# Kernel tuning notes

Hardware: AMD Instinct MI355X
Metric: run time of the kernel (lower is better)

## Reference

```python
import jax, jax.numpy as jnp
import numpy as np

N = 50000      # n_nodes
E = 800000     # edges (before self-loops)
IN = 128       # in_dim
HID = 32       # hidden_dim (per-head out channels)
HEADS = 4
EMB = 128      # embed_dim
LAYERS = 3
NEG_SLOPE = 0.2  # PyG GATv2 default leaky_relu slope


def _layer_norm(x, g, b):
    mu = jnp.mean(x, axis=-1, keepdims=True)
    var = jnp.var(x, axis=-1, keepdims=True)
    return g * (x - mu) / jnp.sqrt(var + 1e-5) + b


def _gatv2(h, src, dst, n, Wl, bl, Wr, br, att, bias):
    # GATv2Conv (PyG semantics, share_weights=False, concat=True).
    H, C = att.shape
    xl = (h @ Wl + bl).reshape(n, H, C)   # target (i) transform
    xr = (h @ Wr + br).reshape(n, H, C)   # source (j) transform
    x_i = xl[dst]                          # [Etot, H, C] gather
    x_j = xr[src]
    e = jax.nn.leaky_relu(x_i + x_j, NEG_SLOPE)
    logit = jnp.einsum('ehc,hc->eh', e, att)          # [Etot, H]
    # segment softmax over destination node (every node has a self-loop)
    m = jax.ops.segment_max(logit, dst, num_segments=n)
    ex = jnp.exp(logit - m[dst])
    den = jax.ops.segment_sum(ex, dst, num_segments=n)
    alpha = ex / (den[dst] + 1e-16)
    out = jax.ops.segment_sum(alpha[..., None] * x_j, dst, num_segments=n)
    return out.reshape(n, H * C) + bias


def setup_inputs() -> dict:
    key = jax.random.key(0)
    ks = iter(jax.random.split(key, 64))
    d = {}
    d['x'] = jax.random.normal(next(ks), (N, IN), jnp.float32)
    d['edge_index'] = jax.random.randint(next(ks), (2, E), 0, N, dtype=jnp.int64)

    def w(shape, fan):
        return jax.random.normal(next(ks), shape, jnp.float32) / np.float32(np.sqrt(fan))

    HC = HID * HEADS
    d['W_in'] = w((IN, HID), IN); d['b_in'] = jnp.zeros((HID,), jnp.float32)
    for i in range(LAYERS):
        ic = HID if i == 0 else HC
        d[f'Wl{i}'] = w((ic, HC), ic); d[f'bl{i}'] = jnp.zeros((HC,), jnp.float32)
        d[f'Wr{i}'] = w((ic, HC), ic); d[f'br{i}'] = jnp.zeros((HC,), jnp.float32)
        d[f'att{i}'] = w((HEADS, HID), HID)
        d[f'bo{i}'] = jnp.zeros((HC,), jnp.float32)
        d[f'g{i}'] = jnp.ones((HC,), jnp.float32)
        d[f'be{i}'] = jnp.zeros((HC,), jnp.float32)
    d['W_out'] = w((HC, EMB), HC); d['b_out'] = jnp.zeros((EMB,), jnp.float32)
    return d


def reference(x, edge_index, W_in, b_in,
              Wl0, bl0, Wr0, br0, att0, bo0, g0, be0,
              Wl1, bl1, Wr1, br1, att1, bo1, g1, be1,
              Wl2, bl2, Wr2, br2, att2, bo2, g2, be2,
              W_out, b_out):
    n = x.shape[0]
    loops = jnp.arange(n, dtype=edge_index.dtype)  # add_self_loops=True
    src = jnp.concatenate([edge_index[0], loops])
    dst = jnp.concatenate([edge_index[1], loops])

    h = jax.nn.gelu(x @ W_in + b_in, approximate=False)
    layers = [(Wl0, bl0, Wr0, br0, att0, bo0, g0, be0),
              (Wl1, bl1, Wr1, br1, att1, bo1, g1, be1),
              (Wl2, bl2, Wr2, br2, att2, bo2, g2, be2)]
    for (Wl, bl, Wr, br, att, bo, g, be) in layers:
        h_new = jax.nn.gelu(_layer_norm(_gatv2(h, src, dst, n, Wl, bl, Wr, br, att, bo), g, be), approximate=False)
        h = h + h_new if h.shape == h_new.shape else h_new  # dropout = identity (eval)
    out = h @ W_out + b_out
    norm = jnp.maximum(jnp.linalg.norm(out, axis=-1, keepdims=True), 1e-12)
    return out / norm
```

## Files before the change

### kernel.cpp

```cpp
#include <hip/hip_runtime.h>
#include <hip/hip_bf16.h>
#include <math.h>

#define N_NODES 50000
#define N_EDGES 800000
#define IN_DIM  128
#define HC_DIM  128
#define HID_C   32
#define SCAN_NB 196
#define LOG2E   1.4426950408889634f

typedef __attribute__((ext_vector_type(8))) short short8;
typedef __attribute__((ext_vector_type(4))) short short4v;
typedef __attribute__((ext_vector_type(4))) float f32x4;
typedef _Float16 hf8 __attribute__((ext_vector_type(8)));
typedef _Float16 hf2 __attribute__((ext_vector_type(2)));
typedef unsigned int uint4v __attribute__((ext_vector_type(4)));

__device__ __forceinline__ float gelu_f(float x){
    return 0.5f*x*(1.0f + erff(x*0.7071067811865475f));
}

__device__ __forceinline__ void split2(float f, short& h, short& l){
    __hip_bfloat16 bh = __float2bfloat16(f);
    float r = f - __bfloat162float(bh);
    __hip_bfloat16 blo = __float2bfloat16(r);
    h = *reinterpret_cast<short*>(&bh);
    l = *reinterpret_cast<short*>(&blo);
}
__device__ __forceinline__ unsigned short f2h(float f){
    _Float16 h = (_Float16)f;
    return __builtin_bit_cast(unsigned short, h);
}

__global__ __launch_bounds__(256) void k_count(const int* __restrict__ dst, int* __restrict__ cnt,
                                               int* __restrict__ rank){
    int b = blockIdx.x*1024 + threadIdx.x;
    #pragma unroll
    for(int i=0;i<4;i++){
        int e = b + i*256;
        if(e < N_EDGES) rank[e] = atomicAdd(&cnt[dst[e]], 1);
    }
}

__global__ __launch_bounds__(256) void k_scan1(const int* __restrict__ cnt, int* __restrict__ rowptr,
                                               int* __restrict__ part){
    __shared__ int sh[256];
    int t=threadIdx.x; int i=blockIdx.x*256+t;
    int v = (i<N_NODES)? cnt[i] : 0;
    sh[t]=v; __syncthreads();
    for(int off=1; off<256; off<<=1){
        int y = (t>=off)? sh[t-off] : 0;
        __syncthreads();
        sh[t] += y;
        __syncthreads();
    }
    if(i<N_NODES) rowptr[i] = sh[t]-v;
    if(t==255) part[blockIdx.x] = sh[255];
}

__global__ __launch_bounds__(256) void k_scan2(int* __restrict__ part){
    __shared__ int sh[256];
    int t=threadIdx.x;
    int v = (t<SCAN_NB)? part[t] : 0;
    sh[t]=v; __syncthreads();
    for(int off=1; off<256; off<<=1){
        int y=(t>=off)? sh[t-off]:0;
        __syncthreads();
        sh[t]+=y;
        __syncthreads();
    }
    if(t<SCAN_NB) part[t] = sh[t]-v;
}

__global__ __launch_bounds__(256) void k_scan3(int* __restrict__ rowptr, const int* __restrict__ part){
    int t=threadIdx.x; int i=blockIdx.x*256+t;
    if(i<N_NODES) rowptr[i] += part[blockIdx.x];
    if(i==0) rowptr[N_NODES]=N_EDGES;
}

__global__ __launch_bounds__(256) void k_fill(const int* __restrict__ src, const int* __restrict__ dst,
                                              const int* __restrict__ rowptr, const int* __restrict__ rank,
                                              int* __restrict__ col){
    int b = blockIdx.x*1024 + threadIdx.x;
    #pragma unroll
    for(int i=0;i<4;i++){
        int e = b + i*256;
        if(e < N_EDGES) col[rowptr[dst[e]] + rank[e]] = src[e];
    }
}

__global__ __launch_bounds__(256) void k_splitW(const float* __restrict__ W0, const float* __restrict__ W1,
                                                const float* __restrict__ W2, const float* __restrict__ W3,
                                                const float* __restrict__ W4, const float* __restrict__ W5,
                                                const float* __restrict__ W6, short* __restrict__ WT){
    int bx = blockIdx.x;
    int m, kc;
    if(bx < 2){ m = bx; kc = 0; }
    else { m = 2 + (bx-2)/4; kc = (bx-2)&3; }
    const float* src; int K; size_t off;
    switch(m){
        case 0: src=W0; K=32;  off=0;      break;
        case 1: src=W1; K=32;  off=8192;   break;
        case 2: src=W2; K=128; off=16384;  break;
        case 3: src=W3; K=128; off=49152;  break;
        case 4: src=W4; K=128; off=81920;  break;
        case 5: src=W5; K=128; off=114688; break;
        default:src=W6; K=128; off=147456; break;
    }
    short* hi = WT + off;
    short* lo = hi + (size_t)K*HC_DIM;
    #pragma unroll
    for(int i=0;i<16;i++){
        int idx = threadIdx.x + i*256;
        int k = kc*32 + (idx>>7);
        int n = idx & 127;
        float f = src[(size_t)k*HC_DIM + n];
        short h,l; split2(f,h,l);
        hi[(size_t)n*K + k] = h;
        lo[(size_t)n*K + k] = l;
    }
}

__global__ __launch_bounds__(256) void k_gemm_in(const float* __restrict__ x, const float* __restrict__ W,
                                                 const float* __restrict__ b, float* __restrict__ h,
                                                 short* __restrict__ hhi, short* __restrict__ hlo){
    int id = blockIdx.x*256+threadIdx.x;
    int r = id>>5, c = id&31;
    const float4* x4 = (const float4*)(x + (size_t)r*IN_DIM);
    float acc=0.f;
    #pragma unroll 8
    for(int k=0;k<IN_DIM/4;k++){
        float4 xv = x4[k];
        acc = fmaf(xv.x, W[(4*k  )*HID_C+c], acc);
        acc = fmaf(xv.y, W[(4*k+1)*HID_C+c], acc);
        acc = fmaf(xv.z, W[(4*k+2)*HID_C+c], acc);
        acc = fmaf(xv.w, W[(4*k+3)*HID_C+c], acc);
    }
    float v = gelu_f(acc + b[c]);
    h[(size_t)r*HID_C+c] = v;
    short hh,ll; split2(v,hh,ll);
    hhi[(size_t)r*HID_C+c] = hh;
    hlo[(size_t)r*HID_C+c] = ll;
}

template<int K, bool PAIR, bool NORM>
__global__ __launch_bounds__(256) void k_mfma(const short* __restrict__ Ahi, const short* __restrict__ Alo,
                                              const short* __restrict__ WTl, const float* __restrict__ bl,
                                              const short* __restrict__ WTr, const float* __restrict__ br,
                                              float* __restrict__ XL, unsigned short* __restrict__ XR16){
    constexpr int LDS_K = 40;
    constexpr int NCH = K / 32;
    __shared__ short As_hi[64*LDS_K], As_lo[64*LDS_K];
    __shared__ short Bh0[128*LDS_K], Bl0[128*LDS_K];
    __shared__ short Bh1[PAIR?128*LDS_K:1], Bl1[PAIR?128*LDS_K:1];
    __shared__ float ssq[NORM?256:1];

    int t = threadIdx.x;
    int lane = t & 63, wave = t >> 6;
    int quad = lane >> 4, ml = lane & 15;
    int rbase = blockIdx.x * 64;

    const short* WTl_lo = WTl + (size_t)K*HC_DIM;
    const short* WTr_lo = PAIR ? (WTr + (size_t)K*HC_DIM) : nullptr;

    f32x4 accL[4][2], accR[4][2];
    #pragma unroll
    for(int i=0;i<4;i++)
        #pragma unroll
        for(int j=0;j<2;j++){ accL[i][j]=(f32x4){0,0,0,0}; accR[i][j]=(f32x4){0,0,0,0}; }

    int r = t >> 2, seg = t & 3;
    int gr = rbase + r; if(gr >= N_NODES) gr = N_NODES-1;

    for(int c=0; c<NCH; c++){
        if(c) __syncthreads();
        size_t ka = (size_t)gr*K + c*32 + seg*8;
        *(short8*)(As_hi + r*LDS_K + seg*8) = *(const short8*)(Ahi + ka);
        *(short8*)(As_lo + r*LDS_K + seg*8) = *(const short8*)(Alo + ka);
        #pragma unroll
        for(int u=0; u<2; u++){
            int uu = t + u*256;
            int n = uu >> 2, sg = uu & 3;
            size_t kw = (size_t)n*K + c*32 + sg*8;
            *(short8*)(Bh0 + n*LDS_K + sg*8) = *(const short8*)(WTl + kw);
            *(short8*)(Bl0 + n*LDS_K + sg*8) = *(const short8*)(WTl_lo + kw);
            if(PAIR){
                *(short8*)(Bh1 + n*LDS_K + sg*8) = *(const short8*)(WTr + kw);
                *(short8*)(Bl1 + n*LDS_K + sg*8) = *(const short8*)(WTr_lo + kw);
            }
        }
        __syncthreads();

        int k0 = quad*8;
        short8 ah[4], al[4];
        #pragma unroll
        for(int i=0;i<4;i++){
            ah[i] = *(const short8*)(As_hi + (16*i + ml)*LDS_K + k0);
            al[i] = *(const short8*)(As_lo + (16*i + ml)*LDS_K + k0);
        }
        #pragma unroll
        for(int j=0;j<2;j++){
            int nrow = j*64 + wave*16 + ml;
            short8 bh = *(const short8*)(Bh0 + nrow*LDS_K + k0);
            short8 blo = *(const short8*)(Bl0 + nrow*LDS_K + k0);
            #pragma unroll
            for(int i=0;i<4;i++){
                accL[i][j] = __builtin_amdgcn_mfma_f32_16x16x32_bf16(ah[i], bh,  accL[i][j], 0,0,0);
                accL[i][j] = __builtin_amdgcn_mfma_f32_16x16x32_bf16(ah[i], blo, accL[i][j], 0,0,0);
                accL[i][j] = __builtin_amdgcn_mfma_f32_16x16x32_bf16(al[i], bh,  accL[i][j], 0,0,0);
            }
            if(PAIR){
                short8 ch = *(const short8*)(Bh1 + nrow*LDS_K + k0);
                short8 cl = *(const short8*)(Bl1 + nrow*LDS_K + k0);
                #pragma unroll
                for(int i=0;i<4;i++){
                    accR[i][j] = __builtin_amdgcn_mfma_f32_16x16x32_bf16(ah[i], ch, accR[i][j], 0,0,0);
                    accR[i][j] = __builtin_amdgcn_mfma_f32_16x16x32_bf16(ah[i], cl, accR[i][j], 0,0,0);
                    accR[i][j] = __builtin_amdgcn_mfma_f32_16x16x32_bf16(al[i], ch, accR[i][j], 0,0,0);
                }
            }
        }
    }

    int col0 = wave*16 + ml, col1 = 64 + wave*16 + ml;
    float bL0 = bl[col0], bL1 = bl[col1];

    if(NORM){
        #pragma unroll
        for(int i=0;i<4;i++){
            #pragma unroll
            for(int rr=0;rr<4;rr++){
                float v0 = accL[i][0][rr] + bL0;
                float v1 = accL[i][1][rr] + bL1;
                float p = v0*v0 + v1*v1;
                p += __shfl_xor(p,1); p += __shfl_xor(p,2);
                p += __shfl_xor(p,4); p += __shfl_xor(p,8);
                if(ml==0) ssq[wave*64 + 16*i + quad*4 + rr] = p;
            }
        }
        __syncthreads();
        #pragma unroll
        for(int i=0;i<4;i++){
            #pragma unroll
            for(int rr=0;rr<4;rr++){
                int row = 16*i + quad*4 + rr;
                int grr = rbase + row;
                if(grr < N_NODES){
                    float tot = ssq[row] + ssq[64+row] + ssq[128+row] + ssq[192+row];
                    float inv = 1.0f / fmaxf(sqrtf(tot), 1e-12f);
                    XL[(size_t)grr*HC_DIM + col0] = (accL[i][0][rr] + bL0) * inv;
                    XL[(size_t)grr*HC_DIM + col1] = (accL[i][1][rr] + bL1) * inv;
                }
            }
        }
    } else {
        float bR0 = PAIR ? br[col0] : 0.f, bR1 = PAIR ? br[col1] : 0.f;
        #pragma unroll
        for(int i=0;i<4;i++){
            #pragma unroll
            for(int rr=0;rr<4;rr++){
                int grr = rbase + 16*i + quad*4 + rr;
                if(grr < N_NODES){
                    XL[(size_t)grr*HC_DIM + col0] = accL[i][0][rr] + bL0;
                    XL[(size_t)grr*HC_DIM + col1] = accL[i][1][rr] + bL1;
                    if(PAIR){
                        XR16[(size_t)grr*HC_DIM + col0] = f2h(accR[i][0][rr] + bR0);
                        XR16[(size_t)grr*HC_DIM + col1] = f2h(accR[i][1][rr] + bR1);
                    }
                }
            }
        }
    }
}

__global__ __launch_bounds__(256) void k_node(const float* __restrict__ XL, const unsigned short* __restrict__ XR,
    const int* __restrict__ rowptr, const int* __restrict__ colidx,
    const float* __restrict__ att, const float* __restrict__ bo,
    const float* __restrict__ gg, const float* __restrict__ be,
    const float* __restrict__ hold, float* __restrict__ hout,
    short* __restrict__ hi_out, short* __restrict__ lo_out)
{
    int wave=threadIdx.x>>6, lane=threadIdx.x&63;
    int node = blockIdx.x*4+wave;
    int qd = lane >> 4, cl = lane & 15;
    int c8 = cl << 3;

    const float* xlp = XL + (size_t)node*HC_DIM + c8;
    float4 xa = *(const float4*)xlp;
    float4 xb = *(const float4*)(xlp+4);
    float xlf[8] = {xa.x,xa.y,xa.z,xa.w,xb.x,xb.y,xb.z,xb.w};
    float4 aa = *(const float4*)(att + c8);
    float4 abv = *(const float4*)(att + c8 + 4);
    float af[8] = {aa.x,aa.y,aa.z,aa.w,abv.x,abv.y,abv.z,abv.w};
    hf8 xlh, av6, av4;
    const float s6 = 0.6f*LOG2E, s4 = 0.4f*LOG2E;
    #pragma unroll
    for(int k=0;k<8;k++){
        xlh[k] = (_Float16)xlf[k];
        av6[k] = (_Float16)(af[k]*s6);
        av4[k] = (_Float16)(af[k]*s4);
    }

    int beg = rowptr[node], end = rowptr[node+1];

    #define H2(v,k) __builtin_shufflevector(v, v, 2*(k), 2*(k)+1)
    #define LOADH(j, xv) { xv = *(const hf8*)((const _Float16*)XR + ((size_t)((unsigned)(j)<<7)) + c8); }
#if defined(__has_builtin) && __has_builtin(__builtin_amdgcn_fdot2)
    #define LOGIT(xv, q) { \
        hf8 u_ = xlh + xv; \
        hf8 a_ = __builtin_bit_cast(hf8, __builtin_bit_cast(uint4v, u_) & 0x7fff7fffu); \
        float qa_ = __builtin_amdgcn_fdot2(H2(u_,0), H2(av6,0), 0.f, false); \
        float qb_ = __builtin_amdgcn_fdot2(H2(a_,0), H2(av4,0), 0.f, false); \
        qa_ = __builtin_amdgcn_fdot2(H2(u_,1), H2(av6,1), qa_, false); \
        qb_ = __builtin_amdgcn_fdot2(H2(a_,1), H2(av4,1), qb_, false); \
        qa_ = __builtin_amdgcn_fdot2(H2(u_,2), H2(av6,2), qa_, false); \
        qb_ = __builtin_amdgcn_fdot2(H2(a_,2), H2(av4,2), qb_, false); \
        qa_ = __builtin_amdgcn_fdot2(H2(u_,3), H2(av6,3), qa_, false); \
        qb_ = __builtin_amdgcn_fdot2(H2(a_,3), H2(av4,3), qb_, false); \
        q = qa_ + qb_; \
        q += __shfl_xor(q,1); q += __shfl_xor(q,2); }
#else
    #define LOGIT(xv, q) { \
        hf8 u_ = xlh + xv; \
        hf8 a_ = __builtin_bit_cast(hf8, __builtin_bit_cast(uint4v, u_) & 0x7fff7fffu); \
        q = 0.f; \
        _Pragma("unroll") \
        for(int k_=0;k_<8;k_++) q = fmaf((float)u_[k_], (float)av6[k_], fmaf((float)a_[k_], (float)av4[k_], q)); \
        q += __shfl_xor(q,1); q += __shfl_xor(q,2); }
#endif
    #define UPDATE4 { \
        float nm = fmaxf(m, fmaxf(fmaxf(q0,q1),fmaxf(q2,q3))); \
        float sc = exp2f(m-nm); \
        float e0=exp2f(q0-nm), e1=exp2f(q1-nm), e2=exp2f(q2-nm), e3=exp2f(q3-nm); \
        ls = fmaf(ls, sc, (e0+e1)+(e2+e3)); \
        _Pragma("unroll") \
        for(int k=0;k<8;k++) \
            acc[k] = fmaf(acc[k], sc, fmaf(e0,(float)x0[k], fmaf(e1,(float)x1[k], fmaf(e2,(float)x2[k], e3*(float)x3[k])))); \
        m = nm; }

    hf8 xs; LOADH(node, xs)
    float qs; LOGIT(xs, qs)
    float m, ls, acc[8];
    if(qd==0){
        m = qs; ls = 1.f;
        #pragma unroll
        for(int k=0;k<8;k++) acc[k] = (float)xs[k];
    } else {
        m = -1e30f; ls = 0.f;
        #pragma unroll
        for(int k=0;k<8;k++) acc[k] = 0.f;
    }

    int P = end - beg;
    int nb = P >> 4;
    int base = beg;
    int qoff = qd << 2;
    for(int b=0; b<nb; b++, base += 16){
        int b2 = base + qoff;
        int j0 = colidx[b2], j1 = colidx[b2+1], j2 = colidx[b2+2], j3 = colidx[b2+3];
        hf8 x0,x1,x2,x3;
        LOADH(j0,x0) LOADH(j1,x1) LOADH(j2,x2) LOADH(j3,x3)
        float q0,q1,q2,q3;
        LOGIT(x0,q0) LOGIT(x1,q1) LOGIT(x2,q2) LOGIT(x3,q3)
        UPDATE4
    }
    if(base < end){
        int b2 = base + qoff;
        int j0 = (b2  <end)? colidx[b2]   : node;
        int j1 = (b2+1<end)? colidx[b2+1] : node;
        int j2 = (b2+2<end)? colidx[b2+2] : node;
        int j3 = (b2+3<end)? colidx[b2+3] : node;
        hf8 x0,x1,x2,x3;
        LOADH(j0,x0) LOADH(j1,x1) LOADH(j2,x2) LOADH(j3,x3)
        float q0,q1,q2,q3;
        LOGIT(x0,q0) LOGIT(x1,q1) LOGIT(x2,q2) LOGIT(x3,q3)
        if(b2+1>=end) q1 = -INFINITY;
        if(b2+2>=end) q2 = -INFINITY;
        if(b2+3>=end) q3 = -INFINITY;
        if(b2 < end){
            UPDATE4
        }
    }
    #undef UPDATE4
    #undef LOGIT
    #undef LOADH
    #undef H2

    #pragma unroll
    for(int mk=16; mk<=32; mk<<=1){
        float mo  = __shfl_xor(m, mk);
        float lso = __shfl_xor(ls, mk);
        float ao[8];
        #pragma unroll
        for(int k=0;k<8;k++) ao[k] = __shfl_xor(acc[k], mk);
        float nm = fmaxf(m, mo);
        float s0 = exp2f(m-nm), s1 = exp2f(mo-nm);
        ls = ls*s0 + lso*s1;
        #pragma unroll
        for(int k=0;k<8;k++) acc[k] = acc[k]*s0 + ao[k]*s1;
        m = nm;
    }

    float inv = 1.0f/ls;
    float4 b0 = *(const float4*)(bo + c8);
    float4 b1 = *(const float4*)(bo + c8 + 4);
    float bof[8] = {b0.x,b0.y,b0.z,b0.w,b1.x,b1.y,b1.z,b1.w};
    float o[8];
    #pragma unroll
    for(int k=0;k<8;k++) o[k] = fmaf(acc[k], inv, bof[k]);
    float s1v = ((o[0]+o[1])+(o[2]+o[3])) + ((o[4]+o[5])+(o[6]+o[7]));
    float s2v = o[0]*o[0];
    #pragma unroll
    for(int k=1;k<8;k++) s2v = fmaf(o[k],o[k],s2v);
    #pragma unroll
    for(int mk=1;mk<16;mk<<=1){ s1v += __shfl_xor(s1v,mk); s2v += __shfl_xor(s2v,mk); }
    float mean = s1v*(1.f/128.f);
    float var  = s2v*(1.f/128.f) - mean*mean;
    float rstd = rsqrtf(var + 1e-5f);

    int ch2 = c8 + (qd<<1);
    float oa = (qd&2) ? ((qd&1)? o[6] : o[4]) : ((qd&1)? o[2] : o[0]);
    float ob = (qd&2) ? ((qd&1)? o[7] : o[5]) : ((qd&1)? o[3] : o[1]);
    float2 g2  = *(const float2*)(gg + ch2);
    float2 be2 = *(const float2*)(be + ch2);
    float r0 = gelu_f(fmaf(g2.x*(oa-mean), rstd, be2.x));
    float r1 = gelu_f(fmaf(g2.y*(ob-mean), rstd, be2.y));
    if(hold){
        float2 hv = *(const float2*)(hold + (size_t)node*HC_DIM + ch2);
        r0 += hv.x; r1 += hv.y;
    }
    *(float2*)(hout + (size_t)node*HC_DIM + ch2) = make_float2(r0,r1);
    short h0,l0,h1,l1;
    split2(r0,h0,l0); split2(r1,h1,l1);
    *(short2*)(hi_out + (size_t)node*HC_DIM + ch2) = make_short2(h0,h1);
    *(short2*)(lo_out + (size_t)node*HC_DIM + ch2) = make_short2(l0,l1);
}

extern "C" void kernel_launch(void* const* d_in, const int* in_sizes, int n_in,
                              void* d_out, int out_size, void* d_ws, size_t ws_size,
                              hipStream_t stream)
{
    const float* x   = (const float*)d_in[0];
    const int*   ei  = (const int*)  d_in[1];
    const float* Win = (const float*)d_in[2];
    const float* bin = (const float*)d_in[3];
    const float *Wl[3], *bl[3], *Wr[3], *br[3], *att[3], *bo[3], *gg[3], *be[3];
    for(int i=0;i<3;i++){
        const int base = 4 + 8*i;
        Wl[i]=(const float*)d_in[base+0]; bl[i]=(const float*)d_in[base+1];
        Wr[i]=(const float*)d_in[base+2]; br[i]=(const float*)d_in[base+3];
        att[i]=(const float*)d_in[base+4]; bo[i]=(const float*)d_in[base+5];
        gg[i]=(const float*)d_in[base+6]; be[i]=(const float*)d_in[base+7];
    }
    const float* Wout=(const float*)d_in[28];
    const float* bout=(const float*)d_in[29];
    float* out = (float*)d_out;

    char* w = (char*)d_ws;
    float* hA = (float*)w;  w += (size_t)N_NODES*HC_DIM*4;
    float* hB = (float*)w;  w += (size_t)N_NODES*HC_DIM*4;
    float* XL = (float*)w;  w += (size_t)N_NODES*HC_DIM*4;
    unsigned short* XR16 = (unsigned short*)w; w += (size_t)N_NODES*HC_DIM*2;
    short* hAhi = (short*)w; w += (size_t)N_NODES*HC_DIM*2;
    short* hAlo = (short*)w; w += (size_t)N_NODES*HC_DIM*2;
    short* hBhi = (short*)w; w += (size_t)N_NODES*HC_DIM*2;
    short* hBlo = (short*)w; w += (size_t)N_NODES*HC_DIM*2;
    short* WT   = (short*)w; w += (size_t)180224*2;
    int* rowptr = (int*)w;  w += (size_t)(N_NODES+2)*4;
    int* cursor = (int*)w;  w += (size_t)N_NODES*4;
    int* colidx = (int*)w;  w += (size_t)N_EDGES*4;
    int* rank   = (int*)w;  w += (size_t)N_EDGES*4;
    int* part   = (int*)w;  w += 256*4;

    const int* srcp = ei;
    const int* dstp = ei + N_EDGES;

    const short* WTl0 = WT + 0;      const short* WTr0 = WT + 8192;
    const short* WTl1 = WT + 16384;  const short* WTr1 = WT + 49152;
    const short* WTl2 = WT + 81920;  const short* WTr2 = WT + 114688;
    const short* WTo  = WT + 147456;

    k_splitW<<<22,256,0,stream>>>(Wl[0],Wr[0],Wl[1],Wr[1],Wl[2],Wr[2],Wout, WT);
    hipMemsetAsync(cursor, 0, (size_t)N_NODES*4, stream);
    k_count <<<782,256, 0, stream>>>(dstp, cursor, rank);
    k_scan1 <<<SCAN_NB,256,0,stream>>>(cursor, rowptr, part);
    k_scan2 <<<1,   256, 0, stream>>>(part);
    k_scan3 <<<SCAN_NB,256,0,stream>>>(rowptr, part);
    k_fill  <<<782,256, 0, stream>>>(srcp, dstp, rowptr, rank, colidx);
    k_gemm_in<<<6250,256,0,stream>>>(x, Win, bin, hA, hAhi, hAlo);

    k_mfma<32,true,false><<<782,256,0,stream>>>(hAhi, hAlo, WTl0, bl[0], WTr0, br[0], XL, XR16);
    k_node<<<12500,256,0,stream>>>(XL,XR16,rowptr,colidx,att[0],bo[0],gg[0],be[0],
                                   (const float*)nullptr, hB, hBhi, hBlo);

    k_mfma<128,true,false><<<782,256,0,stream>>>(hBhi, hBlo, WTl1, bl[1], WTr1, br[1], XL, XR16);
    k_node<<<12500,256,0,stream>>>(XL,XR16,rowptr,colidx,att[1],bo[1],gg[1],be[1], hB, hA, hAhi, hAlo);

    k_mfma<128,true,false><<<782,256,0,stream>>>(hAhi, hAlo, WTl2, bl[2], WTr2, br[2], XL, XR16);
    k_node<<<12500,256,0,stream>>>(XL,XR16,rowptr,colidx,att[2],bo[2],gg[2],be[2], hA, hB, hBhi, hBlo);

    k_mfma<128,false,true><<<782,256,0,stream>>>(hBhi, hBlo, WTo, bout, nullptr, nullptr, out, nullptr);
}
```

Baseline: 496.6 us.

## Drop fp32 hidden buffers, store XL as fp16, add low-degree single-pass softmax path

The fp32 copies of the hidden state are removed. The residual is rebuilt from the bf16 hi/lo split arrays, and the XL projection is written as fp16 instead of fp32, which cuts global writes and reads in every layer. k_node also gets a new path for nodes with fewer than 32 neighbours: it loads up to 8 neighbours per lane at once and runs a non-online softmax, so the gathers overlap better and rescaling is skipped. Storing XL in fp16 adds a small amount of rounding error.

```diff
diff --git a/kernel.cpp b/kernel.cpp
--- a/kernel.cpp
+++ b/kernel.cpp
@@ -31,6 +31,9 @@
 __device__ __forceinline__ unsigned short f2h(float f){
     _Float16 h = (_Float16)f;
     return __builtin_bit_cast(unsigned short, h);
+}
+__device__ __forceinline__ float bf2f(unsigned short u){
+    return __uint_as_float(((unsigned)u)<<16);
 }
 
 __global__ __launch_bounds__(256) void k_count(const int* __restrict__ dst, int* __restrict__ cnt,
@@ -123,7 +126,7 @@
 }
 
 __global__ __launch_bounds__(256) void k_gemm_in(const float* __restrict__ x, const float* __restrict__ W,
-                                                 const float* __restrict__ b, float* __restrict__ h,
+                                                 const float* __restrict__ b,
                                                  short* __restrict__ hhi, short* __restrict__ hlo){
     int id = blockIdx.x*256+threadIdx.x;
     int r = id>>5, c = id&31;
@@ -138,7 +141,6 @@
         acc = fmaf(xv.w, W[(4*k+3)*HID_C+c], acc);
     }
     float v = gelu_f(acc + b[c]);
-    h[(size_t)r*HID_C+c] = v;
     short hh,ll; split2(v,hh,ll);
     hhi[(size_t)r*HID_C+c] = hh;
     hlo[(size_t)r*HID_C+c] = ll;
@@ -148,7 +150,8 @@
 __global__ __launch_bounds__(256) void k_mfma(const short* __restrict__ Ahi, const short* __restrict__ Alo,
                                               const short* __restrict__ WTl, const float* __restrict__ bl,
                                               const short* __restrict__ WTr, const float* __restrict__ br,
-                                              float* __restrict__ XL, unsigned short* __restrict__ XR16){
+                                              float* __restrict__ XLf, unsigned short* __restrict__ XLh,
+                                              unsigned short* __restrict__ XR16){
     constexpr int LDS_K = 40;
     constexpr int NCH = K / 32;
     __shared__ short As_hi[64*LDS_K], As_lo[64*LDS_K];
@@ -249,8 +252,8 @@
                 if(grr < N_NODES){
                     float tot = ssq[row] + ssq[64+row] + ssq[128+row] + ssq[192+row];
                     float inv = 1.0f / fmaxf(sqrtf(tot), 1e-12f);
-                    XL[(size_t)grr*HC_DIM + col0] = (accL[i][0][rr] + bL0) * inv;
-                    XL[(size_t)grr*HC_DIM + col1] = (accL[i][1][rr] + bL1) * inv;
+                    XLf[(size_t)grr*HC_DIM + col0] = (accL[i][0][rr] + bL0) * inv;
+                    XLf[(size_t)grr*HC_DIM + col1] = (accL[i][1][rr] + bL1) * inv;
                 }
             }
         }
@@ -262,8 +265,8 @@
             for(int rr=0;rr<4;rr++){
                 int grr = rbase + 16*i + quad*4 + rr;
                 if(grr < N_NODES){
-                    XL[(size_t)grr*HC_DIM + col0] = accL[i][0][rr] + bL0;
-                    XL[(size_t)grr*HC_DIM + col1] = accL[i][1][rr] + bL1;
+                    XLh[(size_t)grr*HC_DIM + col0] = f2h(accL[i][0][rr] + bL0);
+                    XLh[(size_t)grr*HC_DIM + col1] = f2h(accL[i][1][rr] + bL1);
                     if(PAIR){
                         XR16[(size_t)grr*HC_DIM + col0] = f2h(accR[i][0][rr] + bR0);
                         XR16[(size_t)grr*HC_DIM + col1] = f2h(accR[i][1][rr] + bR1);
@@ -274,35 +277,18 @@
     }
 }
 
-__global__ __launch_bounds__(256) void k_node(const float* __restrict__ XL, const unsigned short* __restrict__ XR,
+__global__ __launch_bounds__(256) void k_node(const unsigned short* __restrict__ XLH, const unsigned short* __restrict__ XR,
     const int* __restrict__ rowptr, const int* __restrict__ colidx,
     const float* __restrict__ att, const float* __restrict__ bo,
     const float* __restrict__ gg, const float* __restrict__ be,
-    const float* __restrict__ hold, float* __restrict__ hout,
+    const short* __restrict__ hold_hi, const short* __restrict__ hold_lo,
     short* __restrict__ hi_out, short* __restrict__ lo_out)
 {
     int wave=threadIdx.x>>6, lane=threadIdx.x&63;
     int node = blockIdx.x*4+wave;
     int qd = lane >> 4, cl = lane & 15;
     int c8 = cl << 3;
-
-    const float* xlp = XL + (size_t)node*HC_DIM + c8;
-    float4 xa = *(const float4*)xlp;
-    float4 xb = *(const float4*)(xlp+4);
-    float xlf[8] = {xa.x,xa.y,xa.z,xa.w,xb.x,xb.y,xb.z,xb.w};
-    float4 aa = *(const float4*)(att + c8);
-    float4 abv = *(const float4*)(att + c8 + 4);
-    float af[8] = {aa.x,aa.y,aa.z,aa.w,abv.x,abv.y,abv.z,abv.w};
-    hf8 xlh, av6, av4;
-    const float s6 = 0.6f*LOG2E, s4 = 0.4f*LOG2E;
-    #pragma unroll
-    for(int k=0;k<8;k++){
-        xlh[k] = (_Float16)xlf[k];
-        av6[k] = (_Float16)(af[k]*s6);
-        av4[k] = (_Float16)(af[k]*s4);
-    }
-
-    int beg = rowptr[node], end = rowptr[node+1];
+    int ch2 = c8 + (qd<<1);
 
     #define H2(v,k) __builtin_shufflevector(v, v, 2*(k), 2*(k)+1)
     #define LOADH(j, xv) { xv = *(const hf8*)((const _Float16*)XR + ((size_t)((unsigned)(j)<<7)) + c8); }
@@ -329,60 +315,124 @@
         for(int k_=0;k_<8;k_++) q = fmaf((float)u_[k_], (float)av6[k_], fmaf((float)a_[k_], (float)av4[k_], q)); \
         q += __shfl_xor(q,1); q += __shfl_xor(q,2); }
 #endif
-    #define UPDATE4 { \
-        float nm = fmaxf(m, fmaxf(fmaxf(q0,q1),fmaxf(q2,q3))); \
-        float sc = exp2f(m-nm); \
-        float e0=exp2f(q0-nm), e1=exp2f(q1-nm), e2=exp2f(q2-nm), e3=exp2f(q3-nm); \
-        ls = fmaf(ls, sc, (e0+e1)+(e2+e3)); \
-        _Pragma("unroll") \
-        for(int k=0;k<8;k++) \
-            acc[k] = fmaf(acc[k], sc, fmaf(e0,(float)x0[k], fmaf(e1,(float)x1[k], fmaf(e2,(float)x2[k], e3*(float)x3[k])))); \
-        m = nm; }
-
+
+    int beg = rowptr[node], end = rowptr[node+1];
+    hf8 xlh = *(const hf8*)((const _Float16*)XLH + ((size_t)((unsigned)node<<7)) + c8);
     hf8 xs; LOADH(node, xs)
+    float hres0 = 0.f, hres1 = 0.f;
+    if(hold_hi){
+        short2 hh = *(const short2*)(hold_hi + (size_t)node*HC_DIM + ch2);
+        short2 hl = *(const short2*)(hold_lo + (size_t)node*HC_DIM + ch2);
+        hres0 = bf2f((unsigned short)hh.x) + bf2f((unsigned short)hl.x);
+        hres1 = bf2f((unsigned short)hh.y) + bf2f((unsigned short)hl.y);
+    }
+
+    float4 aa = *(const float4*)(att + c8);
+    float4 abv = *(const float4*)(att + c8 + 4);
+    float af[8] = {aa.x,aa.y,aa.z,aa.w,abv.x,abv.y,abv.z,abv.w};
+    hf8 av6, av4;
+    const float s6 = 0.6f*LOG2E, s4 = 0.4f*LOG2E;
+    #pragma unroll
+    for(int k=0;k<8;k++){
+        av6[k] = (_Float16)(af[k]*s6);
+        av4[k] = (_Float16)(af[k]*s4);
+    }
+
     float qs; LOGIT(xs, qs)
     float m, ls, acc[8];
-    if(qd==0){
-        m = qs; ls = 1.f;
-        #pragma unroll
-        for(int k=0;k<8;k++) acc[k] = (float)xs[k];
+    int deg = end - beg;
+
+    if(deg < 32){
+        hf8 xv[8]; float q[8];
+        if(deg > 0){
+            int last = end - 1;
+            int qb = beg + (qd<<2);
+            #pragma unroll
+            for(int t=0;t<8;t++){
+                int ii = qb + ((t>>2)<<4) + (t&3);
+                int a = (ii <= last) ? ii : last;
+                int j = colidx[a];
+                LOADH(j, xv[t])
+            }
+            #pragma unroll
+            for(int t=0;t<8;t++){
+                float qq; LOGIT(xv[t], qq)
+                int ii = qb + ((t>>2)<<4) + (t&3);
+                q[t] = (ii <= last) ? qq : -INFINITY;
+            }
+        } else {
+            hf8 z;
+            #pragma unroll
+            for(int k=0;k<8;k++) z[k] = (_Float16)0.f;
+            #pragma unroll
+            for(int t=0;t<8;t++){ xv[t] = z; q[t] = -INFINITY; }
+        }
+        float nm = (qd==0) ? qs : -1e30f;
+        #pragma unroll
+        for(int t=0;t<8;t++) nm = fmaxf(nm, q[t]);
+        float es = (qd==0) ? exp2f(qs-nm) : 0.f;
+        ls = es;
+        #pragma unroll
+        for(int k=0;k<8;k++) acc[k] = es*(float)xs[k];
+        #pragma unroll
+        for(int t=0;t<8;t++){
+            float e = exp2f(q[t]-nm);
+            ls += e;
+            #pragma unroll
+            for(int k=0;k<8;k++) acc[k] = fmaf(e, (float)xv[t][k], acc[k]);
+        }
+        m = nm;
     } else {
-        m = -1e30f; ls = 0.f;
-        #pragma unroll
-        for(int k=0;k<8;k++) acc[k] = 0.f;
-    }
-
-    int P = end - beg;
-    int nb = P >> 4;
-    int base = beg;
-    int qoff = qd << 2;
-    for(int b=0; b<nb; b++, base += 16){
-        int b2 = base + qoff;
-        int j0 = colidx[b2], j1 = colidx[b2+1], j2 = colidx[b2+2], j3 = colidx[b2+3];
-        hf8 x0,x1,x2,x3;
-        LOADH(j0,x0) LOADH(j1,x1) LOADH(j2,x2) LOADH(j3,x3)
-        float q0,q1,q2,q3;
-        LOGIT(x0,q0) LOGIT(x1,q1) LOGIT(x2,q2) LOGIT(x3,q3)
-        UPDATE4
-    }
-    if(base < end){
-        int b2 = base + qoff;
-        int j0 = (b2  <end)? colidx[b2]   : node;
-        int j1 = (b2+1<end)? colidx[b2+1] : node;
-        int j2 = (b2+2<end)? colidx[b2+2] : node;
-        int j3 = (b2+3<end)? colidx[b2+3] : node;
-        hf8 x0,x1,x2,x3;
-        LOADH(j0,x0) LOADH(j1,x1) LOADH(j2,x2) LOADH(j3,x3)
-        float q0,q1,q2,q3;
-        LOGIT(x0,q0) LOGIT(x1,q1) LOGIT(x2,q2) LOGIT(x3,q3)
-        if(b2+1>=end) q1 = -INFINITY;
-        if(b2+2>=end) q2 = -INFINITY;
-        if(b2+3>=end) q3 = -INFINITY;
-        if(b2 < end){
+        #define UPDATE4 { \
+            float nm = fmaxf(m, fmaxf(fmaxf(q0,q1),fmaxf(q2,q3))); \
+            float sc = exp2f(m-nm); \
+            float e0=exp2f(q0-nm), e1=exp2f(q1-nm), e2=exp2f(q2-nm), e3=exp2f(q3-nm); \
+            ls = fmaf(ls, sc, (e0+e1)+(e2+e3)); \
+            _Pragma("unroll") \
+            for(int k=0;k<8;k++) \
+                acc[k] = fmaf(acc[k], sc, fmaf(e0,(float)x0[k], fmaf(e1,(float)x1[k], fmaf(e2,(float)x2[k], e3*(float)x3[k])))); \
+            m = nm; }
+
+        if(qd==0){
+            m = qs; ls = 1.f;
+            #pragma unroll
+            for(int k=0;k<8;k++) acc[k] = (float)xs[k];
+        } else {
+            m = -1e30f; ls = 0.f;
+            #pragma unroll
+            for(int k=0;k<8;k++) acc[k] = 0.f;
+        }
+        int nb = deg >> 4;
+        int base = beg;
+        int qoff = qd << 2;
+        for(int b=0; b<nb; b++, base += 16){
+            int b2 = base + qoff;
+            int j0 = colidx[b2], j1 = colidx[b2+1], j2 = colidx[b2+2], j3 = colidx[b2+3];
+            hf8 x0,x1,x2,x3;
+            LOADH(j0,x0) LOADH(j1,x1) LOADH(j2,x2) LOADH(j3,x3)
+            float q0,q1,q2,q3;
+            LOGIT(x0,q0) LOGIT(x1,q1) LOGIT(x2,q2) LOGIT(x3,q3)
             UPDATE4
         }
-    }
-    #undef UPDATE4
+        if(base < end){
+            int b2 = base + qoff;
+            int j0 = (b2  <end)? colidx[b2]   : node;
+            int j1 = (b2+1<end)? colidx[b2+1] : node;
+            int j2 = (b2+2<end)? colidx[b2+2] : node;
+            int j3 = (b2+3<end)? colidx[b2+3] : node;
+            hf8 x0,x1,x2,x3;
+            LOADH(j0,x0) LOADH(j1,x1) LOADH(j2,x2) LOADH(j3,x3)
+            float q0,q1,q2,q3;
+            LOGIT(x0,q0) LOGIT(x1,q1) LOGIT(x2,q2) LOGIT(x3,q3)
+            if(b2+1>=end) q1 = -INFINITY;
+            if(b2+2>=end) q2 = -INFINITY;
+            if(b2+3>=end) q3 = -INFINITY;
+            if(b2 < end){
+                UPDATE4
+            }
+        }
+        #undef UPDATE4
+    }
     #undef LOGIT
     #undef LOADH
     #undef H2
@@ -419,18 +469,12 @@
     float var  = s2v*(1.f/128.f) - mean*mean;
     float rstd = rsqrtf(var + 1e-5f);
 
-    int ch2 = c8 + (qd<<1);
     float oa = (qd&2) ? ((qd&1)? o[6] : o[4]) : ((qd&1)? o[2] : o[0]);
     float ob = (qd&2) ? ((qd&1)? o[7] : o[5]) : ((qd&1)? o[3] : o[1]);
     float2 g2  = *(const float2*)(gg + ch2);
     float2 be2 = *(const float2*)(be + ch2);
-    float r0 = gelu_f(fmaf(g2.x*(oa-mean), rstd, be2.x));
-    float r1 = gelu_f(fmaf(g2.y*(ob-mean), rstd, be2.y));
-    if(hold){
-        float2 hv = *(const float2*)(hold + (size_t)node*HC_DIM + ch2);
-        r0 += hv.x; r1 += hv.y;
-    }
-    *(float2*)(hout + (size_t)node*HC_DIM + ch2) = make_float2(r0,r1);
+    float r0 = gelu_f(fmaf(g2.x*(oa-mean), rstd, be2.x)) + hres0;
+    float r1 = gelu_f(fmaf(g2.y*(ob-mean), rstd, be2.y)) + hres1;
     short h0,l0,h1,l1;
     split2(r0,h0,l0); split2(r1,h1,l1);
     *(short2*)(hi_out + (size_t)node*HC_DIM + ch2) = make_short2(h0,h1);
@@ -458,9 +502,7 @@
     float* out = (float*)d_out;
 
     char* w = (char*)d_ws;
-    float* hA = (float*)w;  w += (size_t)N_NODES*HC_DIM*4;
-    float* hB = (float*)w;  w += (size_t)N_NODES*HC_DIM*4;
-    float* XL = (float*)w;  w += (size_t)N_NODES*HC_DIM*4;
+    unsigned short* XLH = (unsigned short*)w; w += (size_t)N_NODES*HC_DIM*2;
     unsigned short* XR16 = (unsigned short*)w; w += (size_t)N_NODES*HC_DIM*2;
     short* hAhi = (short*)w; w += (size_t)N_NODES*HC_DIM*2;
     short* hAlo = (short*)w; w += (size_t)N_NODES*HC_DIM*2;
@@ -488,17 +530,23 @@
     k_scan2 <<<1,   256, 0, stream>>>(part);
     k_scan3 <<<SCAN_NB,256,0,stream>>>(rowptr, part);
     k_fill  <<<782,256, 0, stream>>>(srcp, dstp, rowptr, rank, colidx);
-    k_gemm_in<<<6250,256,0,stream>>>(x, Win, bin, hA, hAhi, hAlo);
-
-    k_mfma<32,true,false><<<782,256,0,stream>>>(hAhi, hAlo, WTl0, bl[0], WTr0, br[0], XL, XR16);
-    k_node<<<12500,256,0,stream>>>(XL,XR16,rowptr,colidx,att[0],bo[0],gg[0],be[0],
-                                   (const float*)nullptr, hB, hBhi, hBlo);
-
-    k_mfma<128,true,false><<<782,256,0,stream>>>(hBhi, hBlo, WTl1, bl[1], WTr1, br[1], XL, XR16);
-    k_node<<<12500,256,0,stream>>>(XL,XR16,rowptr,colidx,att[1],bo[1],gg[1],be[1], hB, hA, hAhi, hAlo);
-
-    k_mfma<128,true,false><<<782,256,0,stream>>>(hAhi, hAlo, WTl2, bl[2], WTr2, br[2], XL, XR16);
-    k_node<<<12500,256,0,stream>>>(XL,XR16,rowptr,colidx,att[2],bo[2],gg[2],be[2], hA, hB, hBhi, hBlo);
-
-    k_mfma<128,false,true><<<782,256,0,stream>>>(hBhi, hBlo, WTo, bout, nullptr, nullptr, out, nullptr);
-}
+    k_gemm_in<<<6250,256,0,stream>>>(x, Win, bin, hAhi, hAlo);
+
+    k_mfma<32,true,false><<<782,256,0,stream>>>(hAhi, hAlo, WTl0, bl[0], WTr0, br[0],
+                                                nullptr, XLH, XR16);
+    k_node<<<12500,256,0,stream>>>(XLH,XR16,rowptr,colidx,att[0],bo[0],gg[0],be[0],
+                                   (const short*)nullptr, (const short*)nullptr, hBhi, hBlo);
+
+    k_mfma<128,true,false><<<782,256,0,stream>>>(hBhi, hBlo, WTl1, bl[1], WTr1, br[1],
+                                                 nullptr, XLH, XR16);
+    k_node<<<12500,256,0,stream>>>(XLH,XR16,rowptr,colidx,att[1],bo[1],gg[1],be[1],
+                                   hBhi, hBlo, hAhi, hAlo);
+
+    k_mfma<128,true,false><<<782,256,0,stream>>>(hAhi, hAlo, WTl2, bl[2], WTr2, br[2],
+                                                 nullptr, XLH, XR16);
+    k_node<<<12500,256,0,stream>>>(XLH,XR16,rowptr,colidx,att[2],bo[2],gg[2],be[2],
+                                   hAhi, hAlo, hBhi, hBlo);
+
+    k_mfma<128,false,true><<<782,256,0,stream>>>(hBhi, hBlo, WTo, bout, nullptr, nullptr,
+                                                 out, nullptr, nullptr);
+}
```

Result: slower. 509.2 us (+2.5%).
